# Kernel tuning notes

Hardware: AMD Instinct MI355X
Metric: run time of the kernel (lower is better)

The kernel has to match this reference:

```python
import jax, jax.numpy as jnp
import numpy as np

B, S, H = 8, 2048, 512
M = 4096
TEMP = 0.1
EPS = 1e-6


def setup_inputs() -> dict:
    key = jax.random.key(0)
    ks = jax.random.split(key, 8)
    scale = 1.0 / np.sqrt(H)
    return {
        "hidden_states": jax.random.normal(ks[0], (B, S, H), dtype=jnp.float32),
        "memory_keys": jax.random.normal(ks[1], (M, H), dtype=jnp.float32),
        "memory_values": jax.random.normal(ks[2], (M, H), dtype=jnp.float32),
        "Wk": jax.random.normal(ks[3], (H, H), dtype=jnp.float32) * scale,
        "bk": jnp.zeros((H,), dtype=jnp.float32),
        "Wo": jax.random.normal(ks[4], (H, H), dtype=jnp.float32) * scale,
        "bo": jnp.zeros((H,), dtype=jnp.float32),
        "memory_usage": jax.random.randint(ks[5], (M,), 0, 2, dtype=jnp.int32),
    }


def reference(hidden_states, memory_keys, memory_values, Wk, bk, Wo, bo, memory_usage):
    # key projection: [B,S,H]
    q = jnp.einsum("bsh,kh->bsk", hidden_states, Wk) + bk
    # L2-style normalization with eps inside rsqrt (matches torch.rsqrt(norm_sq + 1e-6))
    q_n = q * jax.lax.rsqrt(jnp.sum(q * q, axis=-1, keepdims=True) + EPS)
    mk_n = memory_keys * jax.lax.rsqrt(
        jnp.sum(memory_keys * memory_keys, axis=-1, keepdims=True) + EPS
    )
    # cosine-similarity scores over the memory bank: [B,S,M]
    scores = jnp.einsum("bsk,mk->bsm", q_n, mk_n) / TEMP
    mask = (memory_usage > 0).astype(scores.dtype)  # [M]
    scores = scores * mask + (-1e9) * (1.0 - mask)
    attn = jax.nn.softmax(scores, axis=-1)  # [B,S,M]
    retrieved = jnp.einsum("bsm,mv->bsv", attn, memory_values)  # [B,S,H]
    out = jnp.einsum("bsv,hv->bsh", retrieved, Wo) + bo
    return out
```

## Files before the change

kernel.cpp:

```cpp
#include <hip/hip_runtime.h>
#include <cstdint>
#include <cstddef>

#define H_DIM   512
#define M_DIM   4096

typedef unsigned short u16;
typedef short bf16x8 __attribute__((ext_vector_type(8)));
typedef float f32x4  __attribute__((ext_vector_type(4)));

__device__ __forceinline__ u16 f2b(float f) {
  union { float f; uint32_t u; } v; v.f = f;
  uint32_t u = v.u + (0x7FFFu + ((v.u >> 16) & 1u));
  return (u16)(u >> 16);
}

__global__ void k_f2bf(const float* __restrict__ in, u16* __restrict__ out, int n4) {
  int i = blockIdx.x * blockDim.x + threadIdx.x;
  if (i < n4) {
    float4 v = ((const float4*)in)[i];
    ushort4 o;
    o.x = f2b(v.x); o.y = f2b(v.y); o.z = f2b(v.z); o.w = f2b(v.w);
    ((ushort4*)out)[i] = o;
  }
}

__global__ void k_f2bf_ww(const float* __restrict__ wk, const float* __restrict__ wo,
                          u16* __restrict__ owk, u16* __restrict__ owo) {
  int i = blockIdx.x * blockDim.x + threadIdx.x;
  const float* src = (i < 65536) ? wk : wo;
  u16* dst = (i < 65536) ? owk : owo;
  int j = i & 65535;
  float4 v = ((const float4*)src)[j];
  ushort4 o;
  o.x = f2b(v.x); o.y = f2b(v.y); o.z = f2b(v.z); o.w = f2b(v.w);
  ((ushort4*)dst)[j] = o;
}

__global__ void k_compact(const int* __restrict__ usage, int* __restrict__ idx,
                          int* __restrict__ meta) {
  __shared__ int cnt[256];
  int t = threadIdx.x;
  int base = t * 16;
  int c = 0;
  #pragma unroll
  for (int i = 0; i < 16; ++i) c += (usage[base + i] > 0) ? 1 : 0;
  cnt[t] = c;
  __syncthreads();
  for (int d = 1; d < 256; d <<= 1) {
    int v = (t >= d) ? cnt[t - d] : 0;
    __syncthreads();
    cnt[t] += v;
    __syncthreads();
  }
  int pos = cnt[t] - c;
  for (int i = 0; i < 16; ++i)
    if (usage[base + i] > 0) idx[pos++] = base + i;
  if (t == 0) {
    int total = cnt[255];
    int keff = ((total + 127) >> 7) << 7;
    meta[0] = total; meta[1] = keff; meta[2] = keff >> 5; meta[3] = keff >> 7;
  }
}

__global__ void k_gather_both(const float* __restrict__ keys, const float* __restrict__ vals,
                              const int* __restrict__ idx, const int* __restrict__ meta,
                              u16* __restrict__ okeys, u16* __restrict__ ovals) {
  int j    = blockIdx.x * 4 + (threadIdx.x >> 6);
  int lane = threadIdx.x & 63;
  int count = meta[0];
  ushort4* kp = (ushort4*)(okeys + (size_t)j * H_DIM);
  ushort4* vp = (ushort4*)(ovals + (size_t)j * H_DIM);
  if (j >= count) {
    ushort4 z = {0, 0, 0, 0};
    kp[lane] = z; kp[lane + 64] = z;
    vp[lane] = z; vp[lane + 64] = z;
    return;
  }
  int src = idx[j];
  const float4* rp = (const float4*)(keys + (size_t)src * H_DIM);
  float4 a = rp[lane];
  float4 b = rp[lane + 64];
  float ss = a.x*a.x + a.y*a.y + a.z*a.z + a.w*a.w
           + b.x*b.x + b.y*b.y + b.z*b.z + b.w*b.w;
  #pragma unroll
  for (int d = 1; d < 64; d <<= 1) ss += __shfl_xor(ss, d, 64);
  float s = rsqrtf(ss + 1e-6f);
  ushort4 oa, ob;
  oa.x = f2b(a.x*s); oa.y = f2b(a.y*s); oa.z = f2b(a.z*s); oa.w = f2b(a.w*s);
  ob.x = f2b(b.x*s); ob.y = f2b(b.y*s); ob.z = f2b(b.z*s); ob.w = f2b(b.w*s);
  kp[lane]      = oa;
  kp[lane + 64] = ob;
  const float4* vr = (const float4*)(vals + (size_t)src * H_DIM);
  float4 c0 = vr[lane];
  float4 c1 = vr[lane + 64];
  ushort4 va, vb;
  va.x = f2b(c0.x); va.y = f2b(c0.y); va.z = f2b(c0.z); va.w = f2b(c0.w);
  vb.x = f2b(c1.x); vb.y = f2b(c1.y); vb.z = f2b(c1.z); vb.w = f2b(c1.w);
  vp[lane]      = va;
  vp[lane + 64] = vb;
}

__global__ void k_rsq(const float* __restrict__ qss, float* __restrict__ rsq) {
  int r = blockIdx.x * blockDim.x + threadIdx.x;
  float s = 0.0f;
  #pragma unroll
  for (int i = 0; i < 8; ++i) s += qss[(size_t)r * 8 + i];
  rsq[r] = rsqrtf(s + 1e-6f);
}

__global__ void k_reduce_l(const float* __restrict__ lpart, float* __restrict__ linv,
                           const int* __restrict__ meta) {
  int r = blockIdx.x * blockDim.x + threadIdx.x;
  int n = meta[1] >> 6;
  float s = 0.0f;
  for (int i = 0; i < n; ++i) s += lpart[(size_t)r * 64 + i];
  linv[r] = 1.0f / s;
}

#define EPI_QPROJ 0
#define EPI_MW    1

template<int EPI>
__global__ __launch_bounds__(256, 3)
void k_gemm_bt(const u16* __restrict__ A, const u16* __restrict__ B,
               int N, int K,
               const int* __restrict__ meta,
               float* __restrict__ outf, u16* __restrict__ outh,
               const float* __restrict__ bias,
               float* __restrict__ aux,
               const float* __restrict__ rowscale) {
  __shared__ u16 Ah[2][128 * 32];
  __shared__ u16 Bh[2][128 * 32];

  const int tid  = threadIdx.x;
  const int wave = tid >> 6, lane = tid & 63;
  const int wr = (wave >> 1) * 64;
  const int wc = (wave & 1) * 64;

  int t0, t_end, t_step, kel, fixedb;
  if (EPI == EPI_QPROJ) {
    fixedb = blockIdx.x; t0 = blockIdx.y; t_end = t0 + 1; t_step = 1; kel = K;
  } else {
    fixedb = blockIdx.y; t0 = blockIdx.x; t_end = meta[1] >> 7; t_step = 16; kel = K;
  }
  const int kiters = kel >> 5;

  const int srow   = lane & 15;
  const int schunk = lane >> 4;
  const int lds_off = schunk * 128 + srow * 8;

  const int fr = lane & 15;
  const int fbase = (lane >> 4) * 128 + fr * 8;
  const int g = lane >> 4;

  const char* Ac = (const char*)A;
  const char* Bc = (const char*)B;

  for (int t = t0; t < t_end; t += t_step) {
    const int row0 = fixedb << 7;
    const int col0 = t << 7;
    __syncthreads();

    uint32_t aB[2], bB[2];
    #pragma unroll
    for (int s2 = 0; s2 < 2; ++s2) {
      aB[s2] = (uint32_t)(((size_t)(row0 + (wave + s2 * 4) * 16 + srow) * (size_t)K
                           + (size_t)(schunk * 8)) * 2u);
      bB[s2] = (uint32_t)(((size_t)(col0 + (wave + s2 * 4) * 16 + srow) * (size_t)K
                           + (size_t)(schunk * 8)) * 2u);
    }

    f32x4 acc[4][4];
    const f32x4 z = {0.0f, 0.0f, 0.0f, 0.0f};
    #pragma unroll
    for (int i = 0; i < 4; ++i)
      #pragma unroll
      for (int j = 0; j < 4; ++j) acc[i][j] = z;

    bf16x8 rA[2], rB[2];
    auto gload = [&](int k0) {
      const uint32_t kb = (uint32_t)(k0 << 1);
      #pragma unroll
      for (int s2 = 0; s2 < 2; ++s2) rA[s2] = *(const bf16x8*)(Ac + aB[s2] + kb);
      #pragma unroll
      for (int s2 = 0; s2 < 2; ++s2) rB[s2] = *(const bf16x8*)(Bc + bB[s2] + kb);
    };

    gload(0);
    for (int it = 0; it < kiters; ++it) {
      const int cur = it & 1;
      #pragma unroll
      for (int s2 = 0; s2 < 2; ++s2)
        *(bf16x8*)&Ah[cur][(wave + s2 * 4) * 512 + lds_off] = rA[s2];
      #pragma unroll
      for (int s2 = 0; s2 < 2; ++s2)
        *(bf16x8*)&Bh[cur][(wave + s2 * 4) * 512 + lds_off] = rB[s2];
      if (it + 1 < kiters) gload((it + 1) << 5);
      __syncthreads();

      bf16x8 af[4], bfv[4];
      #pragma unroll
      for (int i = 0; i < 4; ++i)
        af[i] = *(const bf16x8*)&Ah[cur][((wr >> 4) + i) * 512 + fbase];
      #pragma unroll
      for (int j = 0; j < 4; ++j)
        bfv[j] = *(const bf16x8*)&Bh[cur][((wc >> 4) + j) * 512 + fbase];
      #pragma unroll
      for (int i = 0; i < 4; ++i)
        #pragma unroll
        for (int j = 0; j < 4; ++j)
          acc[i][j] = __builtin_amdgcn_mfma_f32_16x16x32_bf16(af[i], bfv[j], acc[i][j], 0, 0, 0);
    }

    if (EPI == EPI_QPROJ) {
      float sj[4] = {0.f, 0.f, 0.f, 0.f};
      #pragma unroll
      for (int i = 0; i < 4; ++i) {
        const int kb = row0 + wr + i * 16 + g * 4;
        const float4 bkv = *(const float4*)(bias + kb);
        #pragma unroll
        for (int j = 0; j < 4; ++j) {
          const size_t rcol = (size_t)(col0 + wc + j * 16 + fr);
          float v0 = acc[i][j][0] + bkv.x;
          float v1 = acc[i][j][1] + bkv.y;
          float v2 = acc[i][j][2] + bkv.z;
          float v3 = acc[i][j][3] + bkv.w;
          ushort4 st; st.x = f2b(v0); st.y = f2b(v1); st.z = f2b(v2); st.w = f2b(v3);
          *(ushort4*)(outh + rcol * H_DIM + kb) = st;
          sj[j] += v0 * v0 + v1 * v1 + v2 * v2 + v3 * v3;
        }
      }
      const int slot = (row0 + wr) >> 6;
      #pragma unroll
      for (int j = 0; j < 4; ++j) {
        float s = sj[j];
        s += __shfl_xor(s, 16, 64);
        s += __shfl_xor(s, 32, 64);
        if (lane < 16)
          aux[(size_t)(col0 + wc + j * 16 + lane) * 8 + slot] = s;
      }
    } else {
      #pragma unroll
      for (int i = 0; i < 4; ++i) {
        #pragma unroll
        for (int r = 0; r < 4; ++r) {
          int grow = row0 + wr + i * 16 + g * 4 + r;
          #pragma unroll
          for (int j = 0; j < 4; ++j) {
            int gcol = col0 + wc + j * 16 + fr;
            outh[(size_t)grow * (size_t)N + gcol] = f2b(acc[i][j][r]);
          }
        }
      }
    }
  }
}

#define EPI2_P   0
#define EPI2_OUT 1

template<int EPI>
__global__ __launch_bounds__(512, 2)
void k_gemm2(const u16* __restrict__ A, const u16* __restrict__ B,
             const int* __restrict__ meta,
             float* __restrict__ outf, u16* __restrict__ outh,
             const float* __restrict__ bias,
             float* __restrict__ aux,
             const float* __restrict__ rowscale) {
  constexpr int BM  = (EPI == EPI2_P) ? 256 : 128;
  constexpr int MF  = BM / 32;
  constexpr int NF  = 4;
  constexpr int NLA = BM / 128;
  constexpr int NLB = 2;

  __shared__ u16 Ah[2][BM * 32];
  __shared__ u16 Bh[2][256 * 32];

  const int tid  = threadIdx.x;
  const int wave = tid >> 6, lane = tid & 63;
  const int wave_m = wave >> 2, wave_n = wave & 3;
  const int wm0 = wave_m * (BM >> 1);
  const int wn0 = wave_n * 64;
  const int fr  = lane & 15, g = lane >> 4;
  const int fbase = g * 128 + fr * 8;

  int m0, r0, kel;
  if (EPI == EPI2_P) {
    int id = blockIdx.x + (blockIdx.y << 4);
    int xcd = id & 7, s = id >> 3;
    r0 = (xcd * 8 + (s >> 4)) << 8;
    m0 = (s & 15) << 8;
    if (m0 >= meta[1]) return;
    kel = 512;
  } else {
    int id = blockIdx.x + (blockIdx.y << 2);
    int xcd = id & 7, s = id >> 3;
    r0 = (xcd * 8 + (s >> 2)) << 8;
    m0 = (s & 3) << 7;
    kel = meta[1];
  }
  const int kiters = kel >> 5;
  const int kstr = (EPI == EPI2_P) ? 512 : M_DIM;

  const char* Ac = (const char*)A;
  const char* Bc = (const char*)B;
  uint32_t aB[NLA], bB[NLB];
  #pragma unroll
  for (int s2 = 0; s2 < NLA; ++s2) {
    int unit = tid + s2 * 512;
    int row = ((unit >> 6) << 4) + (unit & 15);
    int kch = (unit >> 4) & 3;
    aB[s2] = (uint32_t)(((size_t)(m0 + row) * (size_t)kstr + (size_t)(kch * 8)) * 2u);
  }
  #pragma unroll
  for (int s2 = 0; s2 < NLB; ++s2) {
    int unit = tid + s2 * 512;
    int row = ((unit >> 6) << 4) + (unit & 15);
    int kch = (unit >> 4) & 3;
    bB[s2] = (uint32_t)(((size_t)(r0 + row) * (size_t)kstr + (size_t)(kch * 8)) * 2u);
  }

  f32x4 acc[MF][NF];
  const f32x4 z = {0.0f, 0.0f, 0.0f, 0.0f};
  #pragma unroll
  for (int i = 0; i < MF; ++i)
    #pragma unroll
    for (int j = 0; j < NF; ++j) acc[i][j] = z;

  bf16x8 rA[NLA], rB[NLB];
  auto gload = [&](int k0) {
    const uint32_t kb = (uint32_t)(k0 << 1);
    #pragma unroll
    for (int s2 = 0; s2 < NLA; ++s2) rA[s2] = *(const bf16x8*)(Ac + aB[s2] + kb);
    #pragma unroll
    for (int s2 = 0; s2 < NLB; ++s2) rB[s2] = *(const bf16x8*)(Bc + bB[s2] + kb);
  };

  gload(0);
  for (int it = 0; it < kiters; ++it) {
    const int cur = it & 1;
    #pragma unroll
    for (int s2 = 0; s2 < NLA; ++s2)
      *(bf16x8*)&Ah[cur][(tid + s2 * 512) * 8] = rA[s2];
    #pragma unroll
    for (int s2 = 0; s2 < NLB; ++s2)
      *(bf16x8*)&Bh[cur][(tid + s2 * 512) * 8] = rB[s2];
    if (it + 1 < kiters) gload((it + 1) << 5);
    __syncthreads();

    bf16x8 af[MF], bfv[NF];
    #pragma unroll
    for (int i = 0; i < MF; ++i)
      af[i] = *(const bf16x8*)&Ah[cur][((wm0 >> 4) + i) * 512 + fbase];
    #pragma unroll
    for (int j = 0; j < NF; ++j)
      bfv[j] = *(const bf16x8*)&Bh[cur][((wn0 >> 4) + j) * 512 + fbase];
    #pragma unroll
    for (int i = 0; i < MF; ++i)
      #pragma unroll
      for (int j = 0; j < NF; ++j)
        acc[i][j] = __builtin_amdgcn_mfma_f32_16x16x32_bf16(af[i], bfv[j], acc[i][j], 0, 0, 0);
  }

  if (EPI == EPI2_P) {
    const int count = meta[0];
    float rq10[NF];
    #pragma unroll
    for (int j = 0; j < NF; ++j)
      rq10[j] = rowscale[r0 + wn0 + j * 16 + fr] * 10.0f;
    float sj[NF] = {0.f, 0.f, 0.f, 0.f};
    #pragma unroll
    for (int i = 0; i < MF; ++i) {
      const int mb = m0 + wm0 + i * 16 + g * 4;
      #pragma unroll
      for (int j = 0; j < NF; ++j) {
        const size_t rr = (size_t)(r0 + wn0 + j * 16 + fr);
        float p0 = (mb + 0 < count) ? __expf(acc[i][j][0] * rq10[j]) : 0.0f;
        float p1 = (mb + 1 < count) ? __expf(acc[i][j][1] * rq10[j]) : 0.0f;
        float p2 = (mb + 2 < count) ? __expf(acc[i][j][2] * rq10[j]) : 0.0f;
        float p3 = (mb + 3 < count) ? __expf(acc[i][j][3] * rq10[j]) : 0.0f;
        ushort4 st; st.x = f2b(p0); st.y = f2b(p1); st.z = f2b(p2); st.w = f2b(p3);
        *(ushort4*)(outh + rr * M_DIM + mb) = st;
        sj[j] += (p0 + p1) + (p2 + p3);
      }
    }
    const int slot = (m0 + wm0) >> 6;
    #pragma unroll
    for (int j = 0; j < NF; ++j) {
      float s = sj[j];
      s += __shfl_xor(s, 16, 64);
      s += __shfl_xor(s, 32, 64);
      if (lane < 16) {
        const size_t rr = (size_t)(r0 + wn0 + j * 16 + lane);
        aux[rr * 64 + slot]     = s;
        aux[rr * 64 + slot + 1] = 0.0f;
      }
    }
  } else {
    float scl[NF];
    #pragma unroll
    for (int j = 0; j < NF; ++j)
      scl[j] = rowscale[r0 + wn0 + j * 16 + fr];
    #pragma unroll
    for (int i = 0; i < MF; ++i) {
      const int hb = m0 + wm0 + i * 16 + g * 4;
      const float4 bv = *(const float4*)(bias + hb);
      #pragma unroll
      for (int j = 0; j < NF; ++j) {
        const size_t rr = (size_t)(r0 + wn0 + j * 16 + fr);
        float4 o;
        o.x = acc[i][j][0] * scl[j] + bv.x;
        o.y = acc[i][j][1] * scl[j] + bv.y;
        o.z = acc[i][j][2] * scl[j] + bv.z;
        o.w = acc[i][j][3] * scl[j] + bv.w;
        *(float4*)(outf + rr * H_DIM + hb) = o;
      }
    }
  }
}

extern "C" void kernel_launch(void* const* d_in, const int* in_sizes, int n_in,
                              void* d_out, int out_size, void* d_ws, size_t ws_size,
                              hipStream_t stream) {
  const float* hidden = (const float*)d_in[0];
  const float* mkeys  = (const float*)d_in[1];
  const float* mvals  = (const float*)d_in[2];
  const float* Wk     = (const float*)d_in[3];
  const float* bk     = (const float*)d_in[4];
  const float* Wo     = (const float*)d_in[5];
  const float* bo     = (const float*)d_in[6];
  const int*   usage  = (const int*)d_in[7];
  (void)in_sizes; (void)n_in; (void)out_size; (void)ws_size;

  char* ws = (char*)d_ws;
  u16*   hb    = (u16*)(ws + 0);
  int*   idx   = (int*)(ws + 0);
  int*   meta  = (int*)(ws + 16384);
  float* lpart = (float*)(ws + 1048576);
  u16*   wkb   = (u16*)(ws + 16777216);
  u16*   wob   = (u16*)(ws + 17301504);
  u16*   mkn   = (u16*)(ws + 17825792);
  u16*   mv_c  = (u16*)(ws + 22020096);
  u16*   qb    = (u16*)(ws + 26214400);
  u16*   MWt   = (u16*)(ws + 42991616);
  u16*   P     = (u16*)(ws + 47185920);
  float* qss   = (float*)(ws + 47185920);
  float* rsqQ  = (float*)(ws + 181665792);
  float* linv  = (float*)(ws + 183828480);

  k_f2bf<<<8192, 256, 0, stream>>>(hidden, hb, 2097152);
  k_f2bf_ww<<<512, 256, 0, stream>>>(Wk, Wo, wkb, wob);

  k_gemm_bt<EPI_QPROJ><<<dim3(4, 128), 256, 0, stream>>>(wkb, hb, 512, 512,
      nullptr, nullptr, qb, bk, qss, nullptr);
  k_rsq<<<64, 256, 0, stream>>>(qss, rsqQ);

  k_compact<<<1, 256, 0, stream>>>(usage, idx, meta);
  k_gather_both<<<1024, 256, 0, stream>>>(mkeys, mvals, idx, meta, mkn, mv_c);

  k_gemm_bt<EPI_MW><<<dim3(16, 4), 256, 0, stream>>>(wob, mv_c, M_DIM, 512,
      meta, nullptr, MWt, nullptr, nullptr, nullptr);

  k_gemm2<EPI2_P><<<dim3(16, 64), 512, 0, stream>>>(mkn, qb, meta,
      nullptr, P, nullptr, lpart, rsqQ);
  k_reduce_l<<<64, 256, 0, stream>>>(lpart, linv, meta);

  k_gemm2<EPI2_OUT><<<dim3(4, 64), 512, 0, stream>>>(MWt, P, meta,
      (float*)d_out, nullptr, bo, nullptr, linv);
}
```

Before: 255.1 us.

## Deepen gemm2 K-step to 64 and route Q projection through gemm2

The main GEMM kernel now stages 64-wide K slices per LDS buffer (two 32-wide sub-tiles), which halves the number of barriers per K loop. The next global load is issued after the first fragment reads so it overlaps the MFMA work. The Q projection moves from the 256-thread 128x128 gemm_bt kernel onto this 512-thread 128x256 gemm2 path, with a new epilogue that keeps the bias, bf16 store and per-row sum-of-squares outputs. LDS use doubles, which may reduce occupancy, and every gemm2 K extent must now be a multiple of 64.

Measured after the change: 274.9 us. 1.08x slower.

```diff
diff --git a/kernel.cpp b/kernel.cpp
--- a/kernel.cpp
+++ b/kernel.cpp
@@ -118,7 +118,6 @@
   linv[r] = 1.0f / s;
 }
 
-#define EPI_QPROJ 0
 #define EPI_MW    1
 
 template<int EPI>
@@ -126,10 +125,7 @@
 void k_gemm_bt(const u16* __restrict__ A, const u16* __restrict__ B,
                int N, int K,
                const int* __restrict__ meta,
-               float* __restrict__ outf, u16* __restrict__ outh,
-               const float* __restrict__ bias,
-               float* __restrict__ aux,
-               const float* __restrict__ rowscale) {
+               u16* __restrict__ outh) {
   __shared__ u16 Ah[2][128 * 32];
   __shared__ u16 Bh[2][128 * 32];
 
@@ -138,13 +134,9 @@
   const int wr = (wave >> 1) * 64;
   const int wc = (wave & 1) * 64;
 
-  int t0, t_end, t_step, kel, fixedb;
-  if (EPI == EPI_QPROJ) {
-    fixedb = blockIdx.x; t0 = blockIdx.y; t_end = t0 + 1; t_step = 1; kel = K;
-  } else {
-    fixedb = blockIdx.y; t0 = blockIdx.x; t_end = meta[1] >> 7; t_step = 16; kel = K;
-  }
-  const int kiters = kel >> 5;
+  int t0 = blockIdx.x, t_end = meta[1] >> 7, t_step = 16;
+  int fixedb = blockIdx.y;
+  const int kiters = K >> 5;
 
   const int srow   = lane & 15;
   const int schunk = lane >> 4;
@@ -213,52 +205,24 @@
           acc[i][j] = __builtin_amdgcn_mfma_f32_16x16x32_bf16(af[i], bfv[j], acc[i][j], 0, 0, 0);
     }
 
-    if (EPI == EPI_QPROJ) {
-      float sj[4] = {0.f, 0.f, 0.f, 0.f};
-      #pragma unroll
-      for (int i = 0; i < 4; ++i) {
-        const int kb = row0 + wr + i * 16 + g * 4;
-        const float4 bkv = *(const float4*)(bias + kb);
+    #pragma unroll
+    for (int i = 0; i < 4; ++i) {
+      #pragma unroll
+      for (int r = 0; r < 4; ++r) {
+        int grow = row0 + wr + i * 16 + g * 4 + r;
         #pragma unroll
         for (int j = 0; j < 4; ++j) {
-          const size_t rcol = (size_t)(col0 + wc + j * 16 + fr);
-          float v0 = acc[i][j][0] + bkv.x;
-          float v1 = acc[i][j][1] + bkv.y;
-          float v2 = acc[i][j][2] + bkv.z;
-          float v3 = acc[i][j][3] + bkv.w;
-          ushort4 st; st.x = f2b(v0); st.y = f2b(v1); st.z = f2b(v2); st.w = f2b(v3);
-          *(ushort4*)(outh + rcol * H_DIM + kb) = st;
-          sj[j] += v0 * v0 + v1 * v1 + v2 * v2 + v3 * v3;
+          int gcol = col0 + wc + j * 16 + fr;
+          outh[(size_t)grow * (size_t)N + gcol] = f2b(acc[i][j][r]);
         }
       }
-      const int slot = (row0 + wr) >> 6;
-      #pragma unroll
-      for (int j = 0; j < 4; ++j) {
-        float s = sj[j];
-        s += __shfl_xor(s, 16, 64);
-        s += __shfl_xor(s, 32, 64);
-        if (lane < 16)
-          aux[(size_t)(col0 + wc + j * 16 + lane) * 8 + slot] = s;
-      }
-    } else {
-      #pragma unroll
-      for (int i = 0; i < 4; ++i) {
-        #pragma unroll
-        for (int r = 0; r < 4; ++r) {
-          int grow = row0 + wr + i * 16 + g * 4 + r;
-          #pragma unroll
-          for (int j = 0; j < 4; ++j) {
-            int gcol = col0 + wc + j * 16 + fr;
-            outh[(size_t)grow * (size_t)N + gcol] = f2b(acc[i][j][r]);
-          }
-        }
-      }
-    }
-  }
-}
-
-#define EPI2_P   0
-#define EPI2_OUT 1
+    }
+  }
+}
+
+#define EPI2_P     0
+#define EPI2_OUT   1
+#define EPI2_QPROJ 2
 
 template<int EPI>
 __global__ __launch_bounds__(512, 2)
@@ -268,14 +232,17 @@
              const float* __restrict__ bias,
              float* __restrict__ aux,
              const float* __restrict__ rowscale) {
-  constexpr int BM  = (EPI == EPI2_P) ? 256 : 128;
-  constexpr int MF  = BM / 32;
-  constexpr int NF  = 4;
-  constexpr int NLA = BM / 128;
-  constexpr int NLB = 2;
-
-  __shared__ u16 Ah[2][BM * 32];
-  __shared__ u16 Bh[2][256 * 32];
+  constexpr int BM   = (EPI == EPI2_P) ? 256 : 128;
+  constexpr int MF   = BM / 32;
+  constexpr int NF   = 4;
+  constexpr int APS  = BM / 128;
+  constexpr int NLA  = BM / 64;
+  constexpr int NLB  = 4;
+  constexpr int ASUB = BM * 32;
+  constexpr int BSUB = 256 * 32;
+
+  __shared__ u16 Ah[2][BM * 64];
+  __shared__ u16 Bh[2][256 * 64];
 
   const int tid  = threadIdx.x;
   const int wave = tid >> 6, lane = tid & 63;
@@ -293,32 +260,42 @@
     m0 = (s & 15) << 8;
     if (m0 >= meta[1]) return;
     kel = 512;
+  } else if (EPI == EPI2_OUT) {
+    int id = blockIdx.x + (blockIdx.y << 2);
+    int xcd = id & 7, s = id >> 3;
+    r0 = (xcd * 8 + (s >> 2)) << 8;
+    m0 = (s & 3) << 7;
+    kel = meta[1];
   } else {
     int id = blockIdx.x + (blockIdx.y << 2);
     int xcd = id & 7, s = id >> 3;
     r0 = (xcd * 8 + (s >> 2)) << 8;
     m0 = (s & 3) << 7;
-    kel = meta[1];
-  }
-  const int kiters = kel >> 5;
-  const int kstr = (EPI == EPI2_P) ? 512 : M_DIM;
+    kel = 512;
+  }
+  const int kiters = kel >> 6;
+  const int kstr = (EPI == EPI2_OUT) ? M_DIM : 512;
 
   const char* Ac = (const char*)A;
   const char* Bc = (const char*)B;
   uint32_t aB[NLA], bB[NLB];
   #pragma unroll
   for (int s2 = 0; s2 < NLA; ++s2) {
-    int unit = tid + s2 * 512;
-    int row = ((unit >> 6) << 4) + (unit & 15);
-    int kch = (unit >> 4) & 3;
-    aB[s2] = (uint32_t)(((size_t)(m0 + row) * (size_t)kstr + (size_t)(kch * 8)) * 2u);
+    int ks = s2 / APS;
+    int u  = tid + (s2 % APS) * 512;
+    int row = ((u >> 6) << 4) + (u & 15);
+    int kch = (u >> 4) & 3;
+    aB[s2] = (uint32_t)(((size_t)(m0 + row) * (size_t)kstr
+                         + (size_t)(ks * 32 + kch * 8)) * 2u);
   }
   #pragma unroll
   for (int s2 = 0; s2 < NLB; ++s2) {
-    int unit = tid + s2 * 512;
-    int row = ((unit >> 6) << 4) + (unit & 15);
-    int kch = (unit >> 4) & 3;
-    bB[s2] = (uint32_t)(((size_t)(r0 + row) * (size_t)kstr + (size_t)(kch * 8)) * 2u);
+    int ks = s2 >> 1;
+    int u  = tid + (s2 & 1) * 512;
+    int row = ((u >> 6) << 4) + (u & 15);
+    int kch = (u >> 4) & 3;
+    bB[s2] = (uint32_t)(((size_t)(r0 + row) * (size_t)kstr
+                         + (size_t)(ks * 32 + kch * 8)) * 2u);
   }
 
   f32x4 acc[MF][NF];
@@ -329,8 +306,8 @@
     for (int j = 0; j < NF; ++j) acc[i][j] = z;
 
   bf16x8 rA[NLA], rB[NLB];
-  auto gload = [&](int k0) {
-    const uint32_t kb = (uint32_t)(k0 << 1);
+  auto gload = [&](int it1) {
+    const uint32_t kb = (uint32_t)(it1 << 7);
     #pragma unroll
     for (int s2 = 0; s2 < NLA; ++s2) rA[s2] = *(const bf16x8*)(Ac + aB[s2] + kb);
     #pragma unroll
@@ -342,11 +319,10 @@
     const int cur = it & 1;
     #pragma unroll
     for (int s2 = 0; s2 < NLA; ++s2)
-      *(bf16x8*)&Ah[cur][(tid + s2 * 512) * 8] = rA[s2];
+      *(bf16x8*)&Ah[cur][(s2 / APS) * ASUB + (tid + (s2 % APS) * 512) * 8] = rA[s2];
     #pragma unroll
     for (int s2 = 0; s2 < NLB; ++s2)
-      *(bf16x8*)&Bh[cur][(tid + s2 * 512) * 8] = rB[s2];
-    if (it + 1 < kiters) gload((it + 1) << 5);
+      *(bf16x8*)&Bh[cur][(s2 >> 1) * BSUB + (tid + (s2 & 1) * 512) * 8] = rB[s2];
     __syncthreads();
 
     bf16x8 af[MF], bfv[NF];
@@ -356,6 +332,18 @@
     #pragma unroll
     for (int j = 0; j < NF; ++j)
       bfv[j] = *(const bf16x8*)&Bh[cur][((wn0 >> 4) + j) * 512 + fbase];
+    if (it + 1 < kiters) gload(it + 1);
+    #pragma unroll
+    for (int i = 0; i < MF; ++i)
+      #pragma unroll
+      for (int j = 0; j < NF; ++j)
+        acc[i][j] = __builtin_amdgcn_mfma_f32_16x16x32_bf16(af[i], bfv[j], acc[i][j], 0, 0, 0);
+    #pragma unroll
+    for (int i = 0; i < MF; ++i)
+      af[i] = *(const bf16x8*)&Ah[cur][ASUB + ((wm0 >> 4) + i) * 512 + fbase];
+    #pragma unroll
+    for (int j = 0; j < NF; ++j)
+      bfv[j] = *(const bf16x8*)&Bh[cur][BSUB + ((wn0 >> 4) + j) * 512 + fbase];
     #pragma unroll
     for (int i = 0; i < MF; ++i)
       #pragma unroll
@@ -397,7 +385,7 @@
         aux[rr * 64 + slot + 1] = 0.0f;
       }
     }
-  } else {
+  } else if (EPI == EPI2_OUT) {
     float scl[NF];
     #pragma unroll
     for (int j = 0; j < NF; ++j)
@@ -416,6 +404,33 @@
         o.w = acc[i][j][3] * scl[j] + bv.w;
         *(float4*)(outf + rr * H_DIM + hb) = o;
       }
+    }
+  } else {
+    float sj[NF] = {0.f, 0.f, 0.f, 0.f};
+    #pragma unroll
+    for (int i = 0; i < MF; ++i) {
+      const int kb = m0 + wm0 + i * 16 + g * 4;
+      const float4 bkv = *(const float4*)(bias + kb);
+      #pragma unroll
+      for (int j = 0; j < NF; ++j) {
+        const size_t rr = (size_t)(r0 + wn0 + j * 16 + fr);
+        float v0 = acc[i][j][0] + bkv.x;
+        float v1 = acc[i][j][1] + bkv.y;
+        float v2 = acc[i][j][2] + bkv.z;
+        float v3 = acc[i][j][3] + bkv.w;
+        ushort4 st; st.x = f2b(v0); st.y = f2b(v1); st.z = f2b(v2); st.w = f2b(v3);
+        *(ushort4*)(outh + rr * H_DIM + kb) = st;
+        sj[j] += v0 * v0 + v1 * v1 + v2 * v2 + v3 * v3;
+      }
+    }
+    const int slot = (m0 + wm0) >> 6;
+    #pragma unroll
+    for (int j = 0; j < NF; ++j) {
+      float s = sj[j];
+      s += __shfl_xor(s, 16, 64);
+      s += __shfl_xor(s, 32, 64);
+      if (lane < 16)
+        aux[(size_t)(r0 + wn0 + j * 16 + lane) * 8 + slot] = s;
     }
   }
 }
@@ -452,15 +467,15 @@
   k_f2bf<<<8192, 256, 0, stream>>>(hidden, hb, 2097152);
   k_f2bf_ww<<<512, 256, 0, stream>>>(Wk, Wo, wkb, wob);
 
-  k_gemm_bt<EPI_QPROJ><<<dim3(4, 128), 256, 0, stream>>>(wkb, hb, 512, 512,
-      nullptr, nullptr, qb, bk, qss, nullptr);
+  k_gemm2<EPI2_QPROJ><<<dim3(4, 64), 512, 0, stream>>>(wkb, hb, nullptr,
+      nullptr, qb, bk, qss, nullptr);
   k_rsq<<<64, 256, 0, stream>>>(qss, rsqQ);
 
   k_compact<<<1, 256, 0, stream>>>(usage, idx, meta);
   k_gather_both<<<1024, 256, 0, stream>>>(mkeys, mvals, idx, meta, mkn, mv_c);
 
   k_gemm_bt<EPI_MW><<<dim3(16, 4), 256, 0, stream>>>(wob, mv_c, M_DIM, 512,
-      meta, nullptr, MWt, nullptr, nullptr, nullptr);
+      meta, MWt);
 
   k_gemm2<EPI2_P><<<dim3(16, 64), 512, 0, stream>>>(mkn, qb, meta,
       nullptr, P, nullptr, lpart, rsqQ);
```
